# Optimization experiments

Measured on AMD Instinct MI355X. Metric: run time of the kernel, lower is better.

Reference implementation:

```python
import jax, jax.numpy as jnp
import numpy as np

H = W = 112
SIGMA = 2.0
CROP0, CROP1 = 28, 84


def gaussian_goal_map(goal_pixel, obj_list, obj_num, road_mask):
    """Vectorized version of batch_gaussian_tensor_obj (sigma=2, H=W=112).
    goal_pixel: [B,2] int (col, row) -> xL=goal_pixel[:,1] rows, yL=goal_pixel[:,0] cols.
    obj_list:   [B,M,2] int, per-object (col_for_rowgrid swap as in torch: xo=xy[1], yo=xy[0]).
    obj_num:    [B] int, number of valid objects.
    road_mask:  [B,H,W] int, 0 = off-road.
    Returns [B,H,W] float32.
    """
    rows = jnp.arange(H, dtype=jnp.float32)[:, None]   # [H,1] (torch `x`)
    cols = jnp.arange(W, dtype=jnp.float32)[None, :]   # [1,W] (torch `y`)
    inv2s2 = 1.0 / (2.0 * SIGMA * SIGMA)

    xL = goal_pixel[:, 1].astype(jnp.float32)[:, None, None]  # [B,1,1]
    yL = goal_pixel[:, 0].astype(jnp.float32)[:, None, None]
    goal_g = jnp.exp(-((rows - xL) ** 2 + (cols - yL) ** 2) * inv2s2)  # [B,H,W]

    xo = obj_list[:, :, 1].astype(jnp.float32)[:, :, None, None]  # [B,M,1,1]
    yo = obj_list[:, :, 0].astype(jnp.float32)[:, :, None, None]
    obj_g = jnp.exp(-((rows - xo) ** 2 + (cols - yo) ** 2) * inv2s2)  # [B,M,H,W]
    M = obj_list.shape[1]
    valid = (jnp.arange(M)[None, :] < obj_num[:, None]).astype(jnp.float32)  # [B,M]
    obj_sum = jnp.einsum('bmhw,bm->bhw', obj_g, valid)

    channel = 0.5 + 0.5 * goal_g - 0.5 * obj_sum
    channel = jnp.where(road_mask == 0, 0.0, channel)
    return channel


def mlp(x, w1, b1, w2, b2):
    return jax.nn.relu(x @ w1 + b1) @ w2 + b2


def setup_inputs() -> dict:
    key = jax.random.key(0)
    ks = jax.random.split(key, 12)
    B, M, T = 128, 64, 12
    HID, OUT = 64, 3 * T
    inp = {
        'goal_pixel': jax.random.randint(ks[0], (B, 2), 0, 112, dtype=jnp.int32),
        'obj_list': jax.random.randint(ks[1], (B, M, 2), 0, 112, dtype=jnp.int32),
        'obj_num': jax.random.randint(ks[2], (B,), 0, M, dtype=jnp.int32),
        'road_mask': jax.random.randint(ks[3], (B, H, W), 0, 2, dtype=jnp.int32),
        'goal_logits': jax.random.normal(ks[4], (B, 56, 56), dtype=jnp.float32),
        'target_positions': jax.random.normal(ks[5], (B, T, 2), dtype=jnp.float32),
        'target_yaws': jax.random.normal(ks[6], (B, T, 1), dtype=jnp.float32),
        'w1': jax.random.normal(ks[7], (2, HID), dtype=jnp.float32) * (1.0 / np.sqrt(2.0)),
        'b1': jnp.zeros((HID,), dtype=jnp.float32),
        'w2': jax.random.normal(ks[8], (HID, OUT), dtype=jnp.float32) * (1.0 / np.sqrt(HID)),
        'b2': jnp.zeros((OUT,), dtype=jnp.float32),
    }
    return inp


def reference(goal_pixel, obj_list, obj_num, road_mask, goal_logits,
              target_positions, target_yaws, w1, b1, w2, b2):
    B = goal_pixel.shape[0]
    # motion head: MLP on float goal pixel, MSE vs flattened (positions, yaws)
    trained_traj = mlp(goal_pixel.astype(jnp.float32), w1, b1, w2, b2)  # [B,36]
    target_traj = jnp.concatenate([target_positions, target_yaws], axis=2).reshape(B, -1)
    motion_loss = jnp.mean((trained_traj - target_traj) ** 2)
    # gaussian splat GT map, crop to central 56x56
    gt_map = gaussian_goal_map(goal_pixel, obj_list, obj_num, road_mask)
    gt_map = gt_map[:, CROP0:CROP1, CROP0:CROP1]  # [B,56,56]
    # BCEWithLogits (reduction='none') summed: logaddexp(0,x) - x*t
    bce = jnp.logaddexp(0.0, goal_logits) - goal_logits * gt_map
    aux_loss = jnp.sum(bce)
    loss = motion_loss + aux_loss
    return loss, aux_loss, motion_loss
```

## Files before the change

### kernel.cpp

```cpp
#include <hip/hip_runtime.h>
#include <hip/hip_bf16.h>
#include <math.h>

#define BATCH     128
#define MOBJ      64
#define HFULL     112
#define CROP0     28
#define CROPSZ    56
#define ROWBLKS   4
#define ROWS_PB   14
#define TPB       128
#define HID       64
#define OUTK      36
#define INV2S2    0.125f
#define CULL_R    18

#define WS_MOTION 512

__global__ __launch_bounds__(TPB) void fused_partials(
    const int* __restrict__ goal_pixel,
    const int* __restrict__ obj_list,
    const int* __restrict__ obj_num,
    const int* __restrict__ road_mask,
    const float* __restrict__ goal_logits,
    const float* __restrict__ tpos,
    const float* __restrict__ tyaw,
    const float* __restrict__ w1,
    const float* __restrict__ b1,
    const float* __restrict__ w2,
    const float* __restrict__ b2,
    float* __restrict__ ws)
{
    const int b   = blockIdx.x;
    const int tid = threadIdx.x;

    if (b == BATCH) {
        if (blockIdx.y != 0) return;
        const int bb = tid;
        const float x0 = (float)goal_pixel[bb * 2 + 0];
        const float x1 = (float)goal_pixel[bb * 2 + 1];

        float acc[OUTK];
#pragma unroll
        for (int k = 0; k < OUTK; ++k) acc[k] = b2[k];
        for (int j = 0; j < HID; ++j) {
            float hj = fmaxf(fmaf(x0, w1[j], fmaf(x1, w1[HID + j], b1[j])), 0.0f);
#pragma unroll
            for (int k = 0; k < OUTK; ++k)
                acc[k] = fmaf(hj, w2[j * OUTK + k], acc[k]);
        }
        float err = 0.0f;
#pragma unroll
        for (int k = 0; k < OUTK; ++k) {
            int t = k / 3, c = k - 3 * t;
            float tg = (c < 2) ? tpos[(bb * 12 + t) * 2 + c] : tyaw[bb * 12 + t];
            float d  = acc[k] - tg;
            err = fmaf(d, d, err);
        }
        err *= (1.0f / (BATCH * OUTK));
        for (int off = 32; off > 0; off >>= 1)
            err += __shfl_down(err, off, 64);
        if ((tid & 63) == 0) ws[WS_MOTION + (tid >> 6)] = err;
        return;
    }

    const int row0 = blockIdx.y * ROWS_PB;
    const int rq   = tid / CROPSZ;
    const int w    = tid - rq * CROPSZ;

    __shared__ float s_rowf[MOBJ][16];
    __shared__ float s_xo[MOBJ];
    __shared__ float s_ycol[MOBJ];
    __shared__ float s_red[2];
    __shared__ int   s_cnt;

    const int n = obj_num[b];
    if (tid == 0) s_cnt = 0;
    __syncthreads();

    const int rlo = CROP0 + row0;
    const int rhi = rlo + ROWS_PB - 1;
    if (tid < n) {
        int xo = obj_list[(b * MOBJ + tid) * 2 + 1];
        int yo = obj_list[(b * MOBJ + tid) * 2 + 0];
        if (xo >= rlo - CULL_R && xo <= rhi + CULL_R) {
            int idx = atomicAdd(&s_cnt, 1);
            s_xo[idx]   = (float)xo;
            s_ycol[idx] = (float)yo;
        }
    }
    __syncthreads();
    const int nc = s_cnt;

    for (int i = tid; i < nc * 16; i += TPB) {
        int m  = i >> 4;
        int j  = i & 15;
        int g  = j >> 3;
        int jj = j & 7;
        float v = 0.0f;
        if (jj < 7) {
            float xo = s_xo[m];
            float r  = (float)(rlo + g * 7 + jj);
            float d  = r - xo;
            v = __expf(-d * d * INV2S2);
        }
        s_rowf[m][j] = v;
    }
    __syncthreads();

    float aux = 0.0f;
    if (rq < 2) {
        const float wf = (float)(CROP0 + w);
        const float xL = (float)goal_pixel[b * 2 + 1];
        const float yL = (float)goal_pixel[b * 2 + 0];
        const float dC = wf - yL;
        const float gc = __expf(-dC * dC * INV2S2);

        float acc[8];
#pragma unroll
        for (int i = 0; i < 8; ++i) acc[i] = 0.0f;

        const float4* rowp = (const float4*)&s_rowf[0][rq * 8];
        for (int m = 0; m < nc; ++m) {
            float yo = s_ycol[m];
            float d  = wf - yo;
            float cf = __expf(-d * d * INV2S2);
            float4 r0 = rowp[m * 4];
            float4 r1 = rowp[m * 4 + 1];
            acc[0] = fmaf(r0.x, cf, acc[0]);
            acc[1] = fmaf(r0.y, cf, acc[1]);
            acc[2] = fmaf(r0.z, cf, acc[2]);
            acc[3] = fmaf(r0.w, cf, acc[3]);
            acc[4] = fmaf(r1.x, cf, acc[4]);
            acc[5] = fmaf(r1.y, cf, acc[5]);
            acc[6] = fmaf(r1.z, cf, acc[6]);
            acc[7] = fmaf(r1.w, cf, acc[7]);
        }

#pragma unroll
        for (int i = 0; i < 7; ++i) {
            int   h  = row0 + rq * 7 + i;
            int   gh = CROP0 + h;
            float dr = (float)gh - xL;
            float g  = __expf(-dr * dr * INV2S2) * gc;
            int   rm = road_mask[(b * HFULL + gh) * HFULL + (CROP0 + w)];
            float gt = rm ? (0.5f + 0.5f * g - 0.5f * acc[i]) : 0.0f;
            float x  = goal_logits[(b * CROPSZ + h) * CROPSZ + w];
            float t  = __expf(-fabsf(x));
            float sp = fmaxf(x, 0.0f) + __logf(1.0f + t);
            aux += sp - x * gt;
        }
    }

    for (int off = 32; off > 0; off >>= 1)
        aux += __shfl_down(aux, off, 64);
    const int wid  = tid >> 6;
    if ((tid & 63) == 0) s_red[wid] = aux;
    __syncthreads();
    if (tid == 0)
        ws[b * ROWBLKS + blockIdx.y] = s_red[0] + s_red[1];
}

__global__ __launch_bounds__(256) void reduce_out(
    const float* __restrict__ ws, float* __restrict__ out)
{
    const int t = threadIdx.x;
    float a = ws[t] + ws[t + 256];
    for (int off = 32; off > 0; off >>= 1)
        a += __shfl_down(a, off, 64);
    __shared__ float s[4];
    if ((t & 63) == 0) s[t >> 6] = a;
    __syncthreads();
    if (t == 0) {
        float aux    = s[0] + s[1] + s[2] + s[3];
        float motion = ws[WS_MOTION] + ws[WS_MOTION + 1];
        out[0] = aux + motion;
        out[1] = aux;
        out[2] = motion;
    }
}

extern "C" void kernel_launch(void* const* d_in, const int* in_sizes, int n_in,
                              void* d_out, int out_size, void* d_ws, size_t ws_size,
                              hipStream_t stream) {
    const int*   goal_pixel  = (const int*)d_in[0];
    const int*   obj_list    = (const int*)d_in[1];
    const int*   obj_num     = (const int*)d_in[2];
    const int*   road_mask   = (const int*)d_in[3];
    const float* goal_logits = (const float*)d_in[4];
    const float* target_pos  = (const float*)d_in[5];
    const float* target_yaw  = (const float*)d_in[6];
    const float* w1          = (const float*)d_in[7];
    const float* b1          = (const float*)d_in[8];
    const float* w2          = (const float*)d_in[9];
    const float* b2          = (const float*)d_in[10];
    float* out = (float*)d_out;
    float* ws  = (float*)d_ws;

    dim3 grid1(BATCH + 1, ROWBLKS);
    fused_partials<<<grid1, TPB, 0, stream>>>(
        goal_pixel, obj_list, obj_num, road_mask, goal_logits,
        target_pos, target_yaw, w1, b1, w2, b2, ws);

    reduce_out<<<1, 256, 0, stream>>>(ws, out);
}
```

Before: 94.17 us.

## Fuse final reduction via last-block atomic counter, prefetch loads, ballot compaction

Merges the separate reduce kernel into the main kernel. A global atomic counter picks the last block to finish, and that block does the final sum, which removes one kernel launch. The goal_logits and road_mask loads are also issued before the object culling so their latency overlaps with shared-memory setup. The shared-memory atomic compaction is replaced by a wavefront ballot/popcount prefix. The price is extra threadfence and atomic traffic per block, and a persistent counter that uses modulo to stay correct across repeated launches.

```diff
diff --git a/kernel.cpp b/kernel.cpp
--- a/kernel.cpp
+++ b/kernel.cpp
@@ -1,5 +1,4 @@
 #include <hip/hip_runtime.h>
-#include <hip/hip_bf16.h>
 #include <math.h>
 
 #define BATCH     128
@@ -16,8 +15,11 @@
 #define CULL_R    18
 
 #define WS_MOTION 512
-
-__global__ __launch_bounds__(TPB) void fused_partials(
+#define NBLOCKS   ((BATCH + 1) * ROWBLKS)
+
+__device__ unsigned int g_ctr = 0;
+
+__global__ __launch_bounds__(TPB) void fused_all(
     const int* __restrict__ goal_pixel,
     const int* __restrict__ obj_list,
     const int* __restrict__ obj_num,
@@ -29,154 +31,172 @@
     const float* __restrict__ b1,
     const float* __restrict__ w2,
     const float* __restrict__ b2,
-    float* __restrict__ ws)
+    float* __restrict__ ws,
+    float* __restrict__ out)
 {
     const int b   = blockIdx.x;
     const int tid = threadIdx.x;
-
-    if (b == BATCH) {
-        if (blockIdx.y != 0) return;
-        const int bb = tid;
-        const float x0 = (float)goal_pixel[bb * 2 + 0];
-        const float x1 = (float)goal_pixel[bb * 2 + 1];
-
-        float acc[OUTK];
-#pragma unroll
-        for (int k = 0; k < OUTK; ++k) acc[k] = b2[k];
-        for (int j = 0; j < HID; ++j) {
-            float hj = fmaxf(fmaf(x0, w1[j], fmaf(x1, w1[HID + j], b1[j])), 0.0f);
-#pragma unroll
-            for (int k = 0; k < OUTK; ++k)
-                acc[k] = fmaf(hj, w2[j * OUTK + k], acc[k]);
-        }
-        float err = 0.0f;
-#pragma unroll
-        for (int k = 0; k < OUTK; ++k) {
-            int t = k / 3, c = k - 3 * t;
-            float tg = (c < 2) ? tpos[(bb * 12 + t) * 2 + c] : tyaw[bb * 12 + t];
-            float d  = acc[k] - tg;
-            err = fmaf(d, d, err);
-        }
-        err *= (1.0f / (BATCH * OUTK));
-        for (int off = 32; off > 0; off >>= 1)
-            err += __shfl_down(err, off, 64);
-        if ((tid & 63) == 0) ws[WS_MOTION + (tid >> 6)] = err;
-        return;
-    }
-
-    const int row0 = blockIdx.y * ROWS_PB;
-    const int rq   = tid / CROPSZ;
-    const int w    = tid - rq * CROPSZ;
 
     __shared__ float s_rowf[MOBJ][16];
     __shared__ float s_xo[MOBJ];
     __shared__ float s_ycol[MOBJ];
     __shared__ float s_red[2];
+    __shared__ float s_fin[2];
     __shared__ int   s_cnt;
-
-    const int n = obj_num[b];
-    if (tid == 0) s_cnt = 0;
+    __shared__ int   s_last;
+
+    if (b == BATCH) {
+        if (blockIdx.y == 0) {
+            const int bb = tid;
+            const float x0 = (float)goal_pixel[bb * 2 + 0];
+            const float x1 = (float)goal_pixel[bb * 2 + 1];
+
+            float acc[OUTK];
+#pragma unroll
+            for (int k = 0; k < OUTK; ++k) acc[k] = b2[k];
+            for (int j = 0; j < HID; ++j) {
+                float hj = fmaxf(fmaf(x0, w1[j], fmaf(x1, w1[HID + j], b1[j])), 0.0f);
+#pragma unroll
+                for (int k = 0; k < OUTK; ++k)
+                    acc[k] = fmaf(hj, w2[j * OUTK + k], acc[k]);
+            }
+            float err = 0.0f;
+#pragma unroll
+            for (int k = 0; k < OUTK; ++k) {
+                int t = k / 3, c = k - 3 * t;
+                float tg = (c < 2) ? tpos[(bb * 12 + t) * 2 + c] : tyaw[bb * 12 + t];
+                float d  = acc[k] - tg;
+                err = fmaf(d, d, err);
+            }
+            err *= (1.0f / (BATCH * OUTK));
+            for (int off = 32; off > 0; off >>= 1)
+                err += __shfl_down(err, off, 64);
+            if ((tid & 63) == 0) ws[WS_MOTION + (tid >> 6)] = err;
+        }
+    } else {
+        const int row0 = blockIdx.y * ROWS_PB;
+        const int rq   = tid / CROPSZ;
+        const int w    = tid - rq * CROPSZ;
+        const int rlo  = CROP0 + row0;
+
+        const int n = obj_num[b];
+
+        float xL = 0.0f, yL = 0.0f;
+        float xlog[7];
+        int   rmv[7];
+        if (rq < 2) {
+            xL = (float)goal_pixel[b * 2 + 1];
+            yL = (float)goal_pixel[b * 2 + 0];
+#pragma unroll
+            for (int i = 0; i < 7; ++i) {
+                int h = row0 + rq * 7 + i;
+                xlog[i] = goal_logits[(b * CROPSZ + h) * CROPSZ + w];
+                rmv[i]  = road_mask[(b * HFULL + CROP0 + h) * HFULL + (CROP0 + w)];
+            }
+        }
+
+        if (tid < 64) {
+            int xo = obj_list[(b * MOBJ + tid) * 2 + 1];
+            int yo = obj_list[(b * MOBJ + tid) * 2 + 0];
+            bool keep = (tid < n) &&
+                        (xo >= rlo - CULL_R) &&
+                        (xo <= rlo + ROWS_PB - 1 + CULL_R);
+            unsigned long long mk = __ballot(keep);
+            if (keep) {
+                int idx = (int)__popcll(mk & ((1ull << tid) - 1ull));
+                s_xo[idx]   = (float)xo;
+                s_ycol[idx] = (float)yo;
+            }
+            if (tid == 0) s_cnt = (int)__popcll(mk);
+        }
+        __syncthreads();
+        const int nc = s_cnt;
+
+        for (int i = tid; i < nc * 16; i += TPB) {
+            int m  = i >> 4;
+            int j  = i & 15;
+            int g  = j >> 3;
+            int jj = j & 7;
+            float v = 0.0f;
+            if (jj < 7) {
+                float xo = s_xo[m];
+                float r  = (float)(rlo + g * 7 + jj);
+                float d  = r - xo;
+                v = __expf(-d * d * INV2S2);
+            }
+            s_rowf[m][j] = v;
+        }
+        __syncthreads();
+
+        float aux = 0.0f;
+        if (rq < 2) {
+            const float wf = (float)(CROP0 + w);
+            const float dC = wf - yL;
+            const float gc = __expf(-dC * dC * INV2S2);
+
+            float acc[8];
+#pragma unroll
+            for (int i = 0; i < 8; ++i) acc[i] = 0.0f;
+
+            const float4* rowp = (const float4*)&s_rowf[0][rq * 8];
+            for (int m = 0; m < nc; ++m) {
+                float yo = s_ycol[m];
+                float d  = wf - yo;
+                float cf = __expf(-d * d * INV2S2);
+                float4 r0 = rowp[m * 4];
+                float4 r1 = rowp[m * 4 + 1];
+                acc[0] = fmaf(r0.x, cf, acc[0]);
+                acc[1] = fmaf(r0.y, cf, acc[1]);
+                acc[2] = fmaf(r0.z, cf, acc[2]);
+                acc[3] = fmaf(r0.w, cf, acc[3]);
+                acc[4] = fmaf(r1.x, cf, acc[4]);
+                acc[5] = fmaf(r1.y, cf, acc[5]);
+                acc[6] = fmaf(r1.z, cf, acc[6]);
+                acc[7] = fmaf(r1.w, cf, acc[7]);
+            }
+
+#pragma unroll
+            for (int i = 0; i < 7; ++i) {
+                int   gh = rlo + rq * 7 + i;
+                float dr = (float)gh - xL;
+                float g  = __expf(-dr * dr * INV2S2) * gc;
+                float gt = rmv[i] ? (0.5f + 0.5f * g - 0.5f * acc[i]) : 0.0f;
+                float x  = xlog[i];
+                float t  = __expf(-fabsf(x));
+                float sp = fmaxf(x, 0.0f) + __logf(1.0f + t);
+                aux += sp - x * gt;
+            }
+        }
+
+        for (int off = 32; off > 0; off >>= 1)
+            aux += __shfl_down(aux, off, 64);
+        if ((tid & 63) == 0) s_red[tid >> 6] = aux;
+        __syncthreads();
+        if (tid == 0)
+            ws[b * ROWBLKS + blockIdx.y] = s_red[0] + s_red[1];
+    }
+
+    __threadfence();
     __syncthreads();
-
-    const int rlo = CROP0 + row0;
-    const int rhi = rlo + ROWS_PB - 1;
-    if (tid < n) {
-        int xo = obj_list[(b * MOBJ + tid) * 2 + 1];
-        int yo = obj_list[(b * MOBJ + tid) * 2 + 0];
-        if (xo >= rlo - CULL_R && xo <= rhi + CULL_R) {
-            int idx = atomicAdd(&s_cnt, 1);
-            s_xo[idx]   = (float)xo;
-            s_ycol[idx] = (float)yo;
-        }
+    if (tid == 0) {
+        unsigned int old = atomicAdd(&g_ctr, 1u);
+        s_last = ((old % NBLOCKS) == (NBLOCKS - 1)) ? 1 : 0;
     }
     __syncthreads();
-    const int nc = s_cnt;
-
-    for (int i = tid; i < nc * 16; i += TPB) {
-        int m  = i >> 4;
-        int j  = i & 15;
-        int g  = j >> 3;
-        int jj = j & 7;
-        float v = 0.0f;
-        if (jj < 7) {
-            float xo = s_xo[m];
-            float r  = (float)(rlo + g * 7 + jj);
-            float d  = r - xo;
-            v = __expf(-d * d * INV2S2);
-        }
-        s_rowf[m][j] = v;
-    }
-    __syncthreads();
-
-    float aux = 0.0f;
-    if (rq < 2) {
-        const float wf = (float)(CROP0 + w);
-        const float xL = (float)goal_pixel[b * 2 + 1];
-        const float yL = (float)goal_pixel[b * 2 + 0];
-        const float dC = wf - yL;
-        const float gc = __expf(-dC * dC * INV2S2);
-
-        float acc[8];
-#pragma unroll
-        for (int i = 0; i < 8; ++i) acc[i] = 0.0f;
-
-        const float4* rowp = (const float4*)&s_rowf[0][rq * 8];
-        for (int m = 0; m < nc; ++m) {
-            float yo = s_ycol[m];
-            float d  = wf - yo;
-            float cf = __expf(-d * d * INV2S2);
-            float4 r0 = rowp[m * 4];
-            float4 r1 = rowp[m * 4 + 1];
-            acc[0] = fmaf(r0.x, cf, acc[0]);
-            acc[1] = fmaf(r0.y, cf, acc[1]);
-            acc[2] = fmaf(r0.z, cf, acc[2]);
-            acc[3] = fmaf(r0.w, cf, acc[3]);
-            acc[4] = fmaf(r1.x, cf, acc[4]);
-            acc[5] = fmaf(r1.y, cf, acc[5]);
-            acc[6] = fmaf(r1.z, cf, acc[6]);
-            acc[7] = fmaf(r1.w, cf, acc[7]);
-        }
-
-#pragma unroll
-        for (int i = 0; i < 7; ++i) {
-            int   h  = row0 + rq * 7 + i;
-            int   gh = CROP0 + h;
-            float dr = (float)gh - xL;
-            float g  = __expf(-dr * dr * INV2S2) * gc;
-            int   rm = road_mask[(b * HFULL + gh) * HFULL + (CROP0 + w)];
-            float gt = rm ? (0.5f + 0.5f * g - 0.5f * acc[i]) : 0.0f;
-            float x  = goal_logits[(b * CROPSZ + h) * CROPSZ + w];
-            float t  = __expf(-fabsf(x));
-            float sp = fmaxf(x, 0.0f) + __logf(1.0f + t);
-            aux += sp - x * gt;
-        }
-    }
-
-    for (int off = 32; off > 0; off >>= 1)
-        aux += __shfl_down(aux, off, 64);
-    const int wid  = tid >> 6;
-    if ((tid & 63) == 0) s_red[wid] = aux;
-    __syncthreads();
-    if (tid == 0)
-        ws[b * ROWBLKS + blockIdx.y] = s_red[0] + s_red[1];
-}
-
-__global__ __launch_bounds__(256) void reduce_out(
-    const float* __restrict__ ws, float* __restrict__ out)
-{
-    const int t = threadIdx.x;
-    float a = ws[t] + ws[t + 256];
-    for (int off = 32; off > 0; off >>= 1)
-        a += __shfl_down(a, off, 64);
-    __shared__ float s[4];
-    if ((t & 63) == 0) s[t >> 6] = a;
-    __syncthreads();
-    if (t == 0) {
-        float aux    = s[0] + s[1] + s[2] + s[3];
-        float motion = ws[WS_MOTION] + ws[WS_MOTION + 1];
-        out[0] = aux + motion;
-        out[1] = aux;
-        out[2] = motion;
+    if (s_last) {
+        __threadfence();
+        float a = ws[tid] + ws[tid + 128] + ws[tid + 256] + ws[tid + 384];
+        for (int off = 32; off > 0; off >>= 1)
+            a += __shfl_down(a, off, 64);
+        if ((tid & 63) == 0) s_fin[tid >> 6] = a;
+        __syncthreads();
+        if (tid == 0) {
+            float aux    = s_fin[0] + s_fin[1];
+            float motion = ws[WS_MOTION] + ws[WS_MOTION + 1];
+            out[0] = aux + motion;
+            out[1] = aux;
+            out[2] = motion;
+        }
     }
 }
 
@@ -198,9 +218,7 @@
     float* ws  = (float*)d_ws;
 
     dim3 grid1(BATCH + 1, ROWBLKS);
-    fused_partials<<<grid1, TPB, 0, stream>>>(
+    fused_all<<<grid1, TPB, 0, stream>>>(
         goal_pixel, obj_list, obj_num, road_mask, goal_logits,
-        target_pos, target_yaw, w1, b1, w2, b2, ws);
-
-    reduce_out<<<1, 256, 0, stream>>>(ws, out);
+        target_pos, target_yaw, w1, b1, w2, b2, ws, out);
 }
```

Result: slower. 99.13 us (+5.3%).
